# Optimization experiments

Measured on AMD Instinct MI355X. Metric: run time of the kernel, lower is better.

The kernel has to match this reference:

```python
import jax, jax.numpy as jnp
import numpy as np

# sizes / constants (mirroring the source module's constants)
M, T_SOL, NX, NY = 12, 64, 256, 256
N_TIMES, NOUT = 50, 256
LX, LY_TARGET = 60.0, 75.0
C_CU_TARGET, C_NI_TARGET = 0.001, 0.0001
T_MAX = 200.0
SIGMA, H, DH = 0.25, 4, 8


def setup_inputs() -> dict:
    key = jax.random.key(0)
    ks = jax.random.split(key, 7)
    u = jax.random.uniform(ks[0], (M, 3), dtype=jnp.float32)
    # rows: (Ly in [30,120], c_Cu in [0,0.0029], c_Ni in [0,0.0018])
    params = jnp.stack([30.0 + 90.0 * u[:, 0], 0.0029 * u[:, 1], 0.0018 * u[:, 2]], axis=1)
    c1_src = jax.random.uniform(ks[1], (M, T_SOL, NX, NY), dtype=jnp.float32) * 0.003
    c2_src = jax.random.uniform(ks[2], (M, T_SOL, NX, NY), dtype=jnp.float32) * 0.002
    Wq = jax.random.normal(ks[3], (H * DH, 3), dtype=jnp.float32) * 0.5
    bq = jax.random.normal(ks[4], (H * DH,), dtype=jnp.float32) * 0.1
    Wk = jax.random.normal(ks[5], (H * DH, 3), dtype=jnp.float32) * 0.5
    bk = jax.random.normal(ks[6], (H * DH,), dtype=jnp.float32) * 0.1
    return {"params": params, "c1_src": c1_src, "c2_src": c2_src,
            "Wq": Wq, "bq": bq, "Wk": Wk, "bk": bk}


def _bilinear_resample(xs, ys, vals, xq, yq):
    """RegularGridInterpolator(linear, fill_value=0) on grid (xs[NX], ys[NY]).
    vals: [T, NX, NY]; query is the outer-product grid xq[PX] x yq[PY].
    Separable bilinear -> [T, PX, PY]."""
    ix = jnp.clip(jnp.searchsorted(xs, xq, side='right') - 1, 0, xs.shape[0] - 2)
    tx = (xq - xs[ix]) / (xs[ix + 1] - xs[ix])
    vx = vals[:, ix, :] * (1.0 - tx)[None, :, None] + vals[:, ix + 1, :] * tx[None, :, None]
    iy = jnp.clip(jnp.searchsorted(ys, yq, side='right') - 1, 0, ys.shape[0] - 2)
    ty = (yq - ys[iy]) / (ys[iy + 1] - ys[iy])
    out = vx[:, :, iy] * (1.0 - ty)[None, None, :] + vx[:, :, iy + 1] * ty[None, None, :]
    inb = ((xq >= xs[0]) & (xq <= xs[-1]))[:, None] & ((yq >= ys[0]) & (yq <= ys[-1]))[None, :]
    return jnp.where(inb[None], out, jnp.float32(0.0))


def _forward(params, c1_src, c2_src, Wq, bq, Wk, bk):
    lys, c_cus, c_nis = params[:, 0], params[:, 1], params[:, 2]
    ly_n = (lys - 30.0) / 90.0
    ccu_n = c_cus / 0.0029
    cni_n = c_nis / 0.0018
    p = jnp.stack([ly_n, ccu_n, cni_n], axis=1)                      # [M,3]
    t = jnp.array([[(LY_TARGET - 30.0) / 90.0,
                    C_CU_TARGET / 0.0029,
                    C_NI_TARGET / 0.0018]], dtype=params.dtype)       # [1,3]
    Q = (t @ Wq.T + bq).reshape(1, H, DH)
    K = (p @ Wk.T + bk).reshape(-1, H, DH)
    attn = jnp.einsum('nhd,mhd->nmh', K, Q) / (DH ** 0.5)            # [M,1,H]
    attn_w = jax.nn.softmax(attn, axis=0).mean(axis=2)[:, 0]         # [M]
    dist2 = (((ly_n - t[0, 0]) / SIGMA) ** 2
             + ((ccu_n - t[0, 1]) / SIGMA) ** 2
             + ((cni_n - t[0, 2]) / SIGMA) ** 2)
    sw = jnp.exp(-dist2 / 2.0)
    sw = sw / sw.sum()
    w = attn_w * sw
    w = w / w.sum()                                                  # [M]

    # grids: source x shared; per-solution y grid rescaled to [0, LY_TARGET]
    xs = jnp.linspace(0.0, LX, NX)
    ys_scaled = (jnp.linspace(0.0, 1.0, NY)[None, :] * lys[:, None]) * (LY_TARGET / lys)[:, None]  # [M,NY]
    xq = jnp.linspace(0.0, LX, NOUT)
    yq = jnp.linspace(0.0, LY_TARGET, NOUT)

    times = jnp.linspace(0.0, min(T_MAX, T_MAX), N_TIMES)
    tidx = jnp.clip((times / T_MAX * T_SOL).astype(jnp.int32), 0, T_SOL - 1)  # [T]
    c1_sel = c1_src[:, tidx]                                          # [M,T,NX,NY]
    c2_sel = c2_src[:, tidx]

    res1, res2 = jax.vmap(
        lambda ys, v1, v2: (_bilinear_resample(xs, ys, v1, xq, yq),
                            _bilinear_resample(xs, ys, v2, xq, yq))
    )(ys_scaled, c1_sel, c2_sel)                                      # each [M,T,NOUT,NOUT]

    c1 = jnp.einsum('m,mtij->tij', w, res1)
    c2 = jnp.einsum('m,mtij->tij', w, res2)
    c1 = c1.at[:, :, 0].set(C_CU_TARGET)
    c2 = c2.at[:, :, -1].set(C_NI_TARGET)
    return jnp.stack([c1, c2])                                        # [2,T,NOUT,NOUT]


def reference(params, c1_src, c2_src, Wq, bq, Wk, bk):
    return _forward(params, c1_src, c2_src, Wq, bq, Wk, bk)
```

## Files before the change

kernel.cpp:

```cpp
#include <hip/hip_runtime.h>

#define MM    12
#define TSOL  64
#define NXX   256
#define NYY   256
#define NTT   50
#define NOUTT 256
#define ROWS  4

__device__ int   g_iy[MM * NOUTT];
__device__ float g_w0[MM * NOUTT];
__device__ float g_w1[MM * NOUTT];

__global__ __launch_bounds__(256) void ai_setup_kernel(
    const float* __restrict__ params,
    const float* __restrict__ Wq, const float* __restrict__ bq,
    const float* __restrict__ Wk, const float* __restrict__ bk)
{
    const int k = threadIdx.x;
    const int m = blockIdx.x;

    __shared__ float s_attn[MM][4];
    __shared__ float s_sw[MM];
    __shared__ float s_wm;
    __shared__ float s_ys[NYY];

    if (k < MM) {
        float ly = params[k * 3 + 0];
        float p0 = (ly - 30.0f) / 90.0f;
        float p1 = params[k * 3 + 1] / 0.0029f;
        float p2 = params[k * 3 + 2] / 0.0018f;
        const float t0 = 0.5f;
        const float t1 = 0.001f / 0.0029f;
        const float t2 = 0.0001f / 0.0018f;
        for (int h = 0; h < 4; ++h) {
            float acc = 0.0f;
            for (int d = 0; d < 8; ++d) {
                int o = h * 8 + d;
                float q  = t0 * Wq[o * 3 + 0] + t1 * Wq[o * 3 + 1] + t2 * Wq[o * 3 + 2] + bq[o];
                float kv = p0 * Wk[o * 3 + 0] + p1 * Wk[o * 3 + 1] + p2 * Wk[o * 3 + 2] + bk[o];
                acc += kv * q;
            }
            s_attn[k][h] = acc * 0.35355339059327373f;
        }
        float d0 = (p0 - t0) / 0.25f;
        float d1 = (p1 - t1) / 0.25f;
        float d2 = (p2 - t2) / 0.25f;
        s_sw[k] = expf(-(d0 * d0 + d1 * d1 + d2 * d2) * 0.5f);
    }
    __syncthreads();

    if (k == 0) {
        float aw[MM];
        for (int j = 0; j < MM; ++j) aw[j] = 0.0f;
        for (int h = 0; h < 4; ++h) {
            float mx = s_attn[0][h];
            for (int j = 1; j < MM; ++j) mx = fmaxf(mx, s_attn[j][h]);
            float e[MM]; float sum = 0.0f;
            for (int j = 0; j < MM; ++j) { e[j] = expf(s_attn[j][h] - mx); sum += e[j]; }
            for (int j = 0; j < MM; ++j) aw[j] += e[j] / sum;
        }
        float swsum = 0.0f;
        for (int j = 0; j < MM; ++j) swsum += s_sw[j];
        float wj[MM]; float wsum = 0.0f;
        for (int j = 0; j < MM; ++j) {
            wj[j] = (aw[j] * 0.25f) * (s_sw[j] / swsum);
            wsum += wj[j];
        }
        s_wm = wj[m] / wsum;
    }

    {
        float ly  = params[m * 3 + 0];
        float inv = 75.0f / ly;
        float l01 = (float)k * (1.0f / 255.0f);
        s_ys[k] = (l01 * ly) * inv;
    }
    __syncthreads();

    float w  = s_wm;
    float yq = (float)k * (75.0f / 255.0f);
    int l = 0, r = NYY;
    while (l < r) { int mid = (l + r) >> 1; if (s_ys[mid] <= yq) l = mid + 1; else r = mid; }
    int iy = l - 1;
    iy = iy < 0 ? 0 : (iy > NYY - 2 ? NYY - 2 : iy);
    float ty  = (yq - s_ys[iy]) / (s_ys[iy + 1] - s_ys[iy]);
    bool  inb = (yq >= s_ys[0]) && (yq <= s_ys[NYY - 1]);
    g_iy[m * NOUTT + k] = iy;
    g_w0[m * NOUTT + k] = inb ? w * (1.0f - ty) : 0.0f;
    g_w1[m * NOUTT + k] = inb ? w * ty : 0.0f;
}

__global__ __launch_bounds__(256) void ai_resample_kernel(
    const float* __restrict__ c1, const float* __restrict__ c2,
    float* __restrict__ out)
{
    const int k  = threadIdx.x;
    const int t  = blockIdx.y;
    const int i0 = blockIdx.x * ROWS;
    int tsrc = (t * TSOL) / (NTT - 1);
    if (tsrc > TSOL - 1) tsrc = TSOL - 1;

    int   iy[MM];
    float w0[MM], w1[MM];
#pragma unroll
    for (int m = 0; m < MM; ++m) {
        iy[m] = g_iy[m * NOUTT + k];
        w0[m] = g_w0[m * NOUTT + k];
        w1[m] = g_w1[m * NOUTT + k];
    }

    for (int r = 0; r < ROWS; ++r) {
        int i = i0 + r;
        size_t rowbase = ((size_t)tsrc * NXX + (size_t)i) * NYY;
        float acc1 = 0.0f, acc2 = 0.0f;
#pragma unroll
        for (int m = 0; m < MM; ++m) {
            size_t off = (size_t)m * (TSOL * NXX * NYY) + rowbase + (size_t)iy[m];
            float a0 = c1[off], a1 = c1[off + 1];
            float b0 = c2[off], b1 = c2[off + 1];
            acc1 += w0[m] * a0 + w1[m] * a1;
            acc2 += w0[m] * b0 + w1[m] * b1;
        }
        if (k == 0)         acc1 = 0.001f;
        if (k == NOUTT - 1) acc2 = 0.0001f;
        out[((size_t)t * NOUTT + (size_t)i) * NOUTT + (size_t)k] = acc1;
        out[((size_t)(NTT + t) * NOUTT + (size_t)i) * NOUTT + (size_t)k] = acc2;
    }
}

extern "C" void kernel_launch(void* const* d_in, const int* in_sizes, int n_in,
                              void* d_out, int out_size, void* d_ws, size_t ws_size,
                              hipStream_t stream) {
    const float* params = (const float*)d_in[0];
    const float* c1     = (const float*)d_in[1];
    const float* c2     = (const float*)d_in[2];
    const float* Wq     = (const float*)d_in[3];
    const float* bq     = (const float*)d_in[4];
    const float* Wk     = (const float*)d_in[5];
    const float* bk     = (const float*)d_in[6];
    float* out = (float*)d_out;

    ai_setup_kernel<<<dim3(MM), dim3(256), 0, stream>>>(params, Wq, bq, Wk, bk);
    ai_resample_kernel<<<dim3(NOUTT / ROWS, NTT), dim3(256), 0, stream>>>(c1, c2, out);
}
```

Baseline: 415.2 us.

## Stage source rows into LDS via async global_load_lds before gathering

The resample kernel no longer issues scattered per-thread global gathers across 24 source rows. It now copies whole source rows for two output rows into shared memory with 16-byte global_load_lds transfers, one row per wave per step, then does the bilinear gather from LDS. Rows per block drop from 4 to 2, which doubles the grid. The intent is more coalesced, higher-throughput global traffic and more memory parallelism. The cost is a 48KB LDS footprint per block, which limits occupancy, plus a block-wide barrier.

```diff
diff --git a/kernel.cpp b/kernel.cpp
--- a/kernel.cpp
+++ b/kernel.cpp
@@ -6,7 +6,7 @@
 #define NYY   256
 #define NTT   50
 #define NOUTT 256
-#define ROWS  4
+#define IPB   2
 
 __device__ int   g_iy[MM * NOUTT];
 __device__ float g_w0[MM * NOUTT];
@@ -95,37 +95,61 @@
     const float* __restrict__ c1, const float* __restrict__ c2,
     float* __restrict__ out)
 {
-    const int k  = threadIdx.x;
-    const int t  = blockIdx.y;
-    const int i0 = blockIdx.x * ROWS;
+    __shared__ float s_rows[IPB * 24 * NYY];
+
+    const int tid  = threadIdx.x;
+    const int lane = tid & 63;
+    const int wv   = tid >> 6;
+    const int t    = blockIdx.y;
+    const int i0   = blockIdx.x * IPB;
     int tsrc = (t * TSOL) / (NTT - 1);
     if (tsrc > TSOL - 1) tsrc = TSOL - 1;
 
-    int   iy[MM];
-    float w0[MM], w1[MM];
+    int   iy[MM]; float w0[MM], w1[MM];
 #pragma unroll
     for (int m = 0; m < MM; ++m) {
-        iy[m] = g_iy[m * NOUTT + k];
-        w0[m] = g_w0[m * NOUTT + k];
-        w1[m] = g_w1[m * NOUTT + k];
+        iy[m] = g_iy[m * NOUTT + tid];
+        w0[m] = g_w0[m * NOUTT + tid];
+        w1[m] = g_w1[m * NOUTT + tid];
     }
 
-    for (int r = 0; r < ROWS; ++r) {
-        int i = i0 + r;
-        size_t rowbase = ((size_t)tsrc * NXX + (size_t)i) * NYY;
+#pragma unroll
+    for (int s = 0; s < IPB * 24 / 4; ++s) {
+        int rs  = s * 4 + wv;
+        int r   = rs / 24;
+        int row = rs % 24;
+        int ch  = row / 12;
+        int m   = row % 12;
+        const float* src = ch ? c2 : c1;
+        size_t gbase = ((size_t)(m * TSOL + tsrc) * NXX + (size_t)(i0 + r)) * NYY;
+        const float* gp = src + gbase + (size_t)lane * 4;
+        float* lp = &s_rows[rs * NYY];
+        __builtin_amdgcn_global_load_lds(
+            (const __attribute__((address_space(1))) void*)gp,
+            (__attribute__((address_space(3))) void*)lp,
+            16, 0, 0);
+    }
+    __syncthreads();
+
+#pragma unroll
+    for (int r = 0; r < IPB; ++r) {
+        const float* rowset = &s_rows[r * 24 * NYY];
         float acc1 = 0.0f, acc2 = 0.0f;
 #pragma unroll
         for (int m = 0; m < MM; ++m) {
-            size_t off = (size_t)m * (TSOL * NXX * NYY) + rowbase + (size_t)iy[m];
-            float a0 = c1[off], a1 = c1[off + 1];
-            float b0 = c2[off], b1 = c2[off + 1];
+            const float* r1 = rowset + m * NYY;
+            const float* r2 = rowset + (12 + m) * NYY;
+            int j = iy[m];
+            float a0 = r1[j], a1 = r1[j + 1];
+            float b0 = r2[j], b1 = r2[j + 1];
             acc1 += w0[m] * a0 + w1[m] * a1;
             acc2 += w0[m] * b0 + w1[m] * b1;
         }
-        if (k == 0)         acc1 = 0.001f;
-        if (k == NOUTT - 1) acc2 = 0.0001f;
-        out[((size_t)t * NOUTT + (size_t)i) * NOUTT + (size_t)k] = acc1;
-        out[((size_t)(NTT + t) * NOUTT + (size_t)i) * NOUTT + (size_t)k] = acc2;
+        int i = i0 + r;
+        float o1 = (tid == 0)         ? 0.001f  : acc1;
+        float o2 = (tid == NOUTT - 1) ? 0.0001f : acc2;
+        out[((size_t)t * NOUTT + (size_t)i) * NOUTT + (size_t)tid] = o1;
+        out[((size_t)(NTT + t) * NOUTT + (size_t)i) * NOUTT + (size_t)tid] = o2;
     }
 }
 
@@ -142,5 +166,5 @@
     float* out = (float*)d_out;
 
     ai_setup_kernel<<<dim3(MM), dim3(256), 0, stream>>>(params, Wq, bq, Wk, bk);
-    ai_resample_kernel<<<dim3(NOUTT / ROWS, NTT), dim3(256), 0, stream>>>(c1, c2, out);
+    ai_resample_kernel<<<dim3(NOUTT / IPB, NTT), dim3(256), 0, stream>>>(c1, c2, out);
 }
```

Result: faster. 405.4 us (-2.4%).

## Recast y-resampling as a 3-tap stencil with float4 loads and wave shuffles

Applied to the files above, without the earlier changes.

The setup kernel now folds each output column's gathered interpolation pair into three fixed taps (k-1, k, k+1). This relies on the scaled source y-grid coinciding with the output grid up to rounding, so iy is always k or k-1. The resample kernel gives each wavefront one output row. Each lane loads contiguous float4 chunks of the source rows and uses neighbour shuffles for the edge taps, replacing per-thread gathered scalar loads with fully coalesced vector loads and stores. The risk is that results become wrong if that grid-alignment assumption ever breaks.

```diff
diff --git a/kernel.cpp b/kernel.cpp
--- a/kernel.cpp
+++ b/kernel.cpp
@@ -6,11 +6,10 @@
 #define NYY   256
 #define NTT   50
 #define NOUTT 256
-#define ROWS  4
 
-__device__ int   g_iy[MM * NOUTT];
-__device__ float g_w0[MM * NOUTT];
-__device__ float g_w1[MM * NOUTT];
+__device__ float g_a[MM * NOUTT];
+__device__ float g_b[MM * NOUTT];
+__device__ float g_c[MM * NOUTT];
 
 __global__ __launch_bounds__(256) void ai_setup_kernel(
     const float* __restrict__ params,
@@ -86,47 +85,58 @@
     iy = iy < 0 ? 0 : (iy > NYY - 2 ? NYY - 2 : iy);
     float ty  = (yq - s_ys[iy]) / (s_ys[iy + 1] - s_ys[iy]);
     bool  inb = (yq >= s_ys[0]) && (yq <= s_ys[NYY - 1]);
-    g_iy[m * NOUTT + k] = iy;
-    g_w0[m * NOUTT + k] = inb ? w * (1.0f - ty) : 0.0f;
-    g_w1[m * NOUTT + k] = inb ? w * ty : 0.0f;
+    float w0 = inb ? w * (1.0f - ty) : 0.0f;
+    float w1 = inb ? w * ty : 0.0f;
+    bool sel = (iy == k);
+    g_a[m * NOUTT + k] = sel ? 0.0f : w0;
+    g_b[m * NOUTT + k] = sel ? w0 : w1;
+    g_c[m * NOUTT + k] = sel ? w1 : 0.0f;
 }
 
-__global__ __launch_bounds__(256) void ai_resample_kernel(
+__global__ __launch_bounds__(256, 4) void ai_resample_kernel(
     const float* __restrict__ c1, const float* __restrict__ c2,
     float* __restrict__ out)
 {
-    const int k  = threadIdx.x;
-    const int t  = blockIdx.y;
-    const int i0 = blockIdx.x * ROWS;
+    const int tid  = threadIdx.x;
+    const int lane = tid & 63;
+    const int wv   = tid >> 6;
+    const int t    = blockIdx.y;
+    const int i    = blockIdx.x * 4 + wv;
     int tsrc = (t * TSOL) / (NTT - 1);
     if (tsrc > TSOL - 1) tsrc = TSOL - 1;
 
-    int   iy[MM];
-    float w0[MM], w1[MM];
+    const int kb = lane * 4;
+    float4 o1 = make_float4(0.f, 0.f, 0.f, 0.f);
+    float4 o2 = make_float4(0.f, 0.f, 0.f, 0.f);
+
 #pragma unroll
     for (int m = 0; m < MM; ++m) {
-        iy[m] = g_iy[m * NOUTT + k];
-        w0[m] = g_w0[m * NOUTT + k];
-        w1[m] = g_w1[m * NOUTT + k];
+        const float4 A = *(const float4*)(g_a + m * NOUTT + kb);
+        const float4 B = *(const float4*)(g_b + m * NOUTT + kb);
+        const float4 C = *(const float4*)(g_c + m * NOUTT + kb);
+        size_t base = ((size_t)((m * TSOL + tsrc) * NXX + i)) * NYY + (size_t)kb;
+        float4 x = *(const float4*)(c1 + base);
+        float4 y = *(const float4*)(c2 + base);
+        float xl = __shfl_up(x.w, 1);
+        float xr = __shfl_down(x.x, 1);
+        float yl = __shfl_up(y.w, 1);
+        float yr = __shfl_down(y.x, 1);
+        o1.x += A.x * xl  + B.x * x.x + C.x * x.y;
+        o1.y += A.y * x.x + B.y * x.y + C.y * x.z;
+        o1.z += A.z * x.y + B.z * x.z + C.z * x.w;
+        o1.w += A.w * x.z + B.w * x.w + C.w * xr;
+        o2.x += A.x * yl  + B.x * y.x + C.x * y.y;
+        o2.y += A.y * y.x + B.y * y.y + C.y * y.z;
+        o2.z += A.z * y.y + B.z * y.z + C.z * y.w;
+        o2.w += A.w * y.z + B.w * y.w + C.w * yr;
     }
 
-    for (int r = 0; r < ROWS; ++r) {
-        int i = i0 + r;
-        size_t rowbase = ((size_t)tsrc * NXX + (size_t)i) * NYY;
-        float acc1 = 0.0f, acc2 = 0.0f;
-#pragma unroll
-        for (int m = 0; m < MM; ++m) {
-            size_t off = (size_t)m * (TSOL * NXX * NYY) + rowbase + (size_t)iy[m];
-            float a0 = c1[off], a1 = c1[off + 1];
-            float b0 = c2[off], b1 = c2[off + 1];
-            acc1 += w0[m] * a0 + w1[m] * a1;
-            acc2 += w0[m] * b0 + w1[m] * b1;
-        }
-        if (k == 0)         acc1 = 0.001f;
-        if (k == NOUTT - 1) acc2 = 0.0001f;
-        out[((size_t)t * NOUTT + (size_t)i) * NOUTT + (size_t)k] = acc1;
-        out[((size_t)(NTT + t) * NOUTT + (size_t)i) * NOUTT + (size_t)k] = acc2;
-    }
+    if (lane == 0)  o1.x = 0.001f;
+    if (lane == 63) o2.w = 0.0001f;
+
+    size_t ob = ((size_t)t * NOUTT + (size_t)i) * NOUTT + (size_t)kb;
+    *(float4*)(out + ob) = o1;
+    *(float4*)(out + (size_t)NTT * NOUTT * NOUTT + ob) = o2;
 }
 
 extern "C" void kernel_launch(void* const* d_in, const int* in_sizes, int n_in,
@@ -142,5 +152,5 @@
     float* out = (float*)d_out;
 
     ai_setup_kernel<<<dim3(MM), dim3(256), 0, stream>>>(params, Wq, bq, Wk, bk);
-    ai_resample_kernel<<<dim3(NOUTT / ROWS, NTT), dim3(256), 0, stream>>>(c1, c2, out);
+    ai_resample_kernel<<<dim3(NOUTT / 4, NTT), dim3(256), 0, stream>>>(c1, c2, out);
 }
```

Result: no change. 418.7 us (+0.8%).
